# Optimization experiments

Measured on AMD Instinct MI355X. Metric: run time of the kernel, lower is better.

Reference implementation:

```python
import jax, jax.numpy as jnp
import numpy as np

DS_DIM = 2
N_EXPERTS = 64
N_CLASSES = 26
IMG = 68
BATCH = 8192
FLAT = 1960  # 10 * 14 * 14 after two conv+pool stages


def _conv2d(x, w, b):
    # x: [B, Cin, H, W], w: [Cout, Cin, kh, kw]
    y = jax.lax.conv_general_dilated(
        x, w, window_strides=(1, 1), padding='VALID',
        dimension_numbers=('NCHW', 'OIHW', 'NCHW'))
    return y + b[None, :, None, None]


def _maxpool2(x):
    return jax.lax.reduce_window(
        x, -jnp.inf, jax.lax.max,
        window_dimensions=(1, 1, 2, 2), window_strides=(1, 1, 2, 2),
        padding='VALID')


def setup_inputs() -> dict:
    key = jax.random.key(0)
    ks = jax.random.split(key, 14)
    x = jax.random.normal(ks[0], (BATCH, DS_DIM), dtype=jnp.float32)
    cls_idx = jax.random.randint(ks[1], (BATCH,), 0, N_CLASSES)
    images = jax.random.normal(ks[2], (N_CLASSES, 1, IMG, IMG), dtype=jnp.float32)
    s = 0.05
    conv1_w = jax.random.normal(ks[3], (5, 1, 5, 5), dtype=jnp.float32) * s
    conv1_b = jax.random.normal(ks[4], (5,), dtype=jnp.float32) * s
    conv2_w = jax.random.normal(ks[5], (10, 5, 5, 5), dtype=jnp.float32) * s
    conv2_b = jax.random.normal(ks[6], (10,), dtype=jnp.float32) * s
    fc1_w = jax.random.normal(ks[7], (500, FLAT + DS_DIM), dtype=jnp.float32) * s
    fc1_b = jax.random.normal(ks[8], (500,), dtype=jnp.float32) * s
    fc2_w = jax.random.normal(ks[9], (N_EXPERTS, 500), dtype=jnp.float32) * s
    fc2_b = jax.random.normal(ks[10], (N_EXPERTS,), dtype=jnp.float32) * s
    # geotorch-constrained expert matrices: B_A positive-semidefinite, C_A skew
    raw_b = jax.random.normal(ks[11], (N_EXPERTS, DS_DIM, DS_DIM), dtype=jnp.float32)
    A_B = jnp.einsum('nik,njk->nij', raw_b, raw_b) * 0.1        # PSD
    raw_c = jax.random.normal(ks[12], (N_EXPERTS, DS_DIM, DS_DIM), dtype=jnp.float32)
    A_C = (raw_c - jnp.swapaxes(raw_c, -1, -2)) * 0.5            # skew
    x_tar = jax.random.normal(ks[13], (1, DS_DIM), dtype=jnp.float32)
    return {'x': x, 'cls_idx': cls_idx, 'images': images,
            'conv1_w': conv1_w, 'conv1_b': conv1_b,
            'conv2_w': conv2_w, 'conv2_b': conv2_b,
            'fc1_w': fc1_w, 'fc1_b': fc1_b,
            'fc2_w': fc2_w, 'fc2_b': fc2_b,
            'A_B': A_B, 'A_C': A_C, 'x_tar': x_tar}


def reference(x, cls_idx, images, conv1_w, conv1_b, conv2_w, conv2_b,
              fc1_w, fc1_b, fc2_w, fc2_b, A_B, A_C, x_tar):
    # gating CNN: gather per-sample image by class index
    img = images[cls_idx]                             # [B, 1, 68, 68]
    h = _maxpool2(jax.nn.relu(_conv2d(img, conv1_w, conv1_b)))   # [B, 5, 32, 32]
    h = _maxpool2(jax.nn.relu(_conv2d(h, conv2_w, conv2_b)))     # [B, 10, 14, 14]
    h = h.reshape(h.shape[0], -1)                     # [B, 1960]
    h = jnp.concatenate([h, x], axis=1)               # [B, 1962]
    h = jax.nn.relu(h @ fc1_w.T + fc1_b)              # [B, 500]
    w_all = jax.nn.softmax(h @ fc2_w.T + fc2_b, axis=1)  # [B, N]
    # fused expert weighted-sum (original: python loop over N tiny matmuls)
    A = A_B + A_C                                     # [N, d, d]
    diff = x_tar - x                                  # [B, d]
    s_all = jnp.einsum('bn,nij,bj->bi', w_all, A, diff)
    return s_all
```

## Files before the change

### kernel.cpp

```cpp
#include <hip/hip_runtime.h>

#define WS_SC1    0
#define WS_FEAT   133120
#define WS_FC1P   184080
#define WS_FC2P   197080
#define WS_AFLAT  229080
#define WS_WX     229336

__global__ __launch_bounds__(256) void k_conv1(
    const float* __restrict__ images, const float* __restrict__ c1w,
    const float* __restrict__ c1b, const float* __restrict__ fc2w,
    const float* __restrict__ fc1w, const float* __restrict__ A_B,
    const float* __restrict__ A_C, float* __restrict__ ws)
{
    const int b = blockIdx.x, t = threadIdx.x;
    if (b >= 520) {
        if (b == 520) {
            float* P = ws + WS_FC2P;
            for (int i = t; i < 8000; i += 256) {
                int j4 = i >> 6, e = i & 63;
                float4 v;
                v.x = fc2w[e * 500 + 4 * j4 + 0];
                v.y = fc2w[e * 500 + 4 * j4 + 1];
                v.z = fc2w[e * 500 + 4 * j4 + 2];
                v.w = fc2w[e * 500 + 4 * j4 + 3];
                *(float4*)&P[i * 4] = v;
            }
        } else {
            float* Af = ws + WS_AFLAT;
            if (t < 256) Af[t] = A_B[t] + A_C[t];
            float* Wx = ws + WS_WX;
            for (int i = t; i < 1000; i += 256) {
                int j = i >> 1, k = i & 1;
                Wx[i] = fc1w[j * 1962 + 1960 + k];
            }
            float* fp = ws + WS_FC1P;
            for (int i = t; i < 13000; i += 256) fp[i] = 0.f;
        }
        return;
    }

    const int c = b / 20, r = b - c * 20;
    const int oc = r >> 2, g = r & 3;
    const int py = g * 8 + (t >> 5), px = t & 31;

    float wr[25];
#pragma unroll
    for (int i = 0; i < 25; ++i) wr[i] = c1w[oc * 25 + i];
    const float bias = c1b[oc];

    const float* im = images + c * 4624 + (2 * py) * 68 + 2 * px;
    float ir[6][6];
#pragma unroll
    for (int a = 0; a < 6; ++a)
#pragma unroll
        for (int q = 0; q < 3; ++q) {
            float2 v = *(const float2*)&im[a * 68 + 2 * q];
            ir[a][2 * q] = v.x; ir[a][2 * q + 1] = v.y;
        }

    float a00 = bias, a01 = bias, a10 = bias, a11 = bias;
#pragma unroll
    for (int ky = 0; ky < 5; ++ky)
#pragma unroll
        for (int kx = 0; kx < 5; ++kx) {
            float w = wr[ky * 5 + kx];
            a00 += w * ir[ky][kx];     a01 += w * ir[ky][kx + 1];
            a10 += w * ir[ky + 1][kx]; a11 += w * ir[ky + 1][kx + 1];
        }
    float v = fmaxf(fmaxf(fmaxf(a00, a01), fmaxf(a10, a11)), 0.f);
    ws[WS_SC1 + ((c * 5 + oc) * 32 + py) * 32 + px] = v;
}

__global__ __launch_bounds__(256) void k_conv2(
    const float* __restrict__ c2w, const float* __restrict__ c2b,
    float* __restrict__ ws)
{
    const int b = blockIdx.x, t = threadIdx.x;
    const int c = b / 10, oc = b - c * 10;

    __shared__ float sw[125];
    if (t < 125) sw[t] = c2w[oc * 125 + t];
    __syncthreads();
    if (t >= 196) return;

    const int py = t / 14, px = t - py * 14;
    const float bias = c2b[oc];
    float a00 = bias, a01 = bias, a10 = bias, a11 = bias;

    const float* base = ws + WS_SC1 + c * 5120 + (2 * py) * 32 + 2 * px;
#pragma unroll
    for (int ic = 0; ic < 5; ++ic) {
        const float* s1 = base + ic * 1024;
        float ir[6][6];
#pragma unroll
        for (int a = 0; a < 6; ++a)
#pragma unroll
            for (int q = 0; q < 3; ++q) {
                float2 v = *(const float2*)&s1[a * 32 + 2 * q];
                ir[a][2 * q] = v.x; ir[a][2 * q + 1] = v.y;
            }
#pragma unroll
        for (int ky = 0; ky < 5; ++ky)
#pragma unroll
            for (int kx = 0; kx < 5; ++kx) {
                float w = sw[ic * 25 + ky * 5 + kx];
                a00 += w * ir[ky][kx];     a01 += w * ir[ky][kx + 1];
                a10 += w * ir[ky + 1][kx]; a11 += w * ir[ky + 1][kx + 1];
            }
    }
    float v = fmaxf(fmaxf(fmaxf(a00, a01), fmaxf(a10, a11)), 0.f);
    ws[WS_FEAT + c * 1960 + oc * 196 + py * 14 + px] = v;
}

__global__ __launch_bounds__(256) void k_fc1(
    const float* __restrict__ fc1w, const float* __restrict__ fc1b,
    float* __restrict__ ws)
{
    const int lane = threadIdx.x & 63, w = threadIdx.x >> 6;
    const int jg = blockIdx.x >> 1, half = blockIdx.x & 1;
    const int j = jg * 4 + w;
    const int kbase = half * 980;

    float wreg[16];
#pragma unroll
    for (int i = 0; i < 16; ++i) {
        int kl = lane + 64 * i;
        wreg[i] = (kl < 980) ? fc1w[j * 1962 + kbase + kl] : 0.f;
    }
    const float bj = (half == 0) ? fc1b[j] : 0.f;
    const float* feat = ws + WS_FEAT;
    float* fc1p = ws + WS_FC1P;

    for (int c = 0; c < 26; ++c) {
        const float* f = feat + c * 1960 + kbase;
        float acc0 = 0.f, acc1 = 0.f;
#pragma unroll
        for (int i = 0; i < 16; i += 2) {
            int k0 = lane + 64 * i, k1 = lane + 64 * (i + 1);
            acc0 += wreg[i]     * f[(k0 < 980) ? k0 : 0];
            acc1 += wreg[i + 1] * f[(k1 < 980) ? k1 : 0];
        }
        float acc = acc0 + acc1;
#pragma unroll
        for (int off = 32; off >= 1; off >>= 1) acc += __shfl_xor(acc, off);
        if (lane == 0) atomicAdd(&fc1p[c * 500 + j], acc + bj);
    }
}

__global__ __launch_bounds__(256) void k_moe(
    const float* __restrict__ x, const int* __restrict__ cls,
    const float* __restrict__ fc2b, const float* __restrict__ x_tar,
    const float* __restrict__ ws, float* __restrict__ out)
{
    __shared__ float sh[8][500];
    __shared__ float sred[2048];
    const int t = threadIdx.x;
    const int b0 = blockIdx.x * 8;
    const float* fc1p = ws + WS_FC1P;
    const float* fc2P = ws + WS_FC2P;
    const float* Af   = ws + WS_AFLAT;
    const float* Wx   = ws + WS_WX;

    int cs[8]; float xs0[8], xs1[8];
#pragma unroll
    for (int s = 0; s < 8; ++s) {
        cs[s]  = cls[b0 + s];
        xs0[s] = x[2 * (b0 + s)];
        xs1[s] = x[2 * (b0 + s) + 1];
    }
    for (int j = t; j < 500; j += 256) {
        float2 wx = *(const float2*)&Wx[2 * j];
#pragma unroll
        for (int s = 0; s < 8; ++s) {
            float v = fc1p[cs[s] * 500 + j] + xs0[s] * wx.x + xs1[s] * wx.y;
            sh[s][j] = fmaxf(v, 0.f);
        }
    }
    __syncthreads();

    const int e = t & 63, p = t >> 6;
    float acc[8];
#pragma unroll
    for (int s = 0; s < 8; ++s) acc[s] = 0.f;

    const int gbeg = p * 32;
    const int gend = (p == 3) ? 125 : (gbeg + 32);
    for (int j4 = gbeg; j4 < gend; ++j4) {
        float4 wv = *(const float4*)&fc2P[(j4 * 64 + e) * 4];
#pragma unroll
        for (int s = 0; s < 8; ++s) {
            float4 h4 = *(const float4*)&sh[s][j4 * 4];
            acc[s] += h4.x * wv.x + h4.y * wv.y + h4.z * wv.z + h4.w * wv.w;
        }
    }
#pragma unroll
    for (int s = 0; s < 8; ++s) sred[p * 512 + s * 64 + e] = acc[s];
    __syncthreads();

    const float xt0 = x_tar[0], xt1 = x_tar[1];
    const float be = fc2b[e];
    const float4 a4 = *(const float4*)&Af[4 * e];
#pragma unroll
    for (int half = 0; half < 2; ++half) {
        int s = half * 4 + p;
        float logit = be + sred[s * 64 + e] + sred[512 + s * 64 + e]
                    + sred[1024 + s * 64 + e] + sred[1536 + s * 64 + e];
        float m = logit;
#pragma unroll
        for (int off = 32; off >= 1; off >>= 1) m = fmaxf(m, __shfl_xor(m, off));
        float ex = __expf(logit - m);
        float sum = ex;
        float m0 = ex * a4.x, m1 = ex * a4.y, m2 = ex * a4.z, m3 = ex * a4.w;
#pragma unroll
        for (int off = 32; off >= 1; off >>= 1) {
            sum += __shfl_xor(sum, off);
            m0 += __shfl_xor(m0, off);
            m1 += __shfl_xor(m1, off);
            m2 += __shfl_xor(m2, off);
            m3 += __shfl_xor(m3, off);
        }
        if (e == 0) {
            int b = b0 + s;
            float d0 = xt0 - x[2 * b], d1 = xt1 - x[2 * b + 1];
            float inv = 1.f / sum;
            out[2 * b]     = (m0 * d0 + m1 * d1) * inv;
            out[2 * b + 1] = (m2 * d0 + m3 * d1) * inv;
        }
    }
}

extern "C" void kernel_launch(void* const* d_in, const int* in_sizes, int n_in,
                              void* d_out, int out_size, void* d_ws, size_t ws_size,
                              hipStream_t stream) {
    const float* x      = (const float*)d_in[0];
    const int*   cls    = (const int*)  d_in[1];
    const float* images = (const float*)d_in[2];
    const float* c1w    = (const float*)d_in[3];
    const float* c1b    = (const float*)d_in[4];
    const float* c2w    = (const float*)d_in[5];
    const float* c2b    = (const float*)d_in[6];
    const float* fc1w   = (const float*)d_in[7];
    const float* fc1b   = (const float*)d_in[8];
    const float* fc2w   = (const float*)d_in[9];
    const float* fc2b   = (const float*)d_in[10];
    const float* A_B    = (const float*)d_in[11];
    const float* A_C    = (const float*)d_in[12];
    const float* x_tar  = (const float*)d_in[13];
    float* out = (float*)d_out;
    float* ws  = (float*)d_ws;

    k_conv1<<<522, 256, 0, stream>>>(images, c1w, c1b, fc2w, fc1w, A_B, A_C, ws);
    k_conv2<<<260, 256, 0, stream>>>(c2w, c2b, ws);
    k_fc1  <<<250, 256, 0, stream>>>(fc1w, fc1b, ws);
    k_moe  <<<1024, 256, 0, stream>>>(x, cls, fc2b, x_tar, ws, out);
}
```

Baseline: 136.2 us.

## Fuse conv1, conv2 and fc1 into one persistent kernel with grid barriers

Merges the three preprocessing kernels into a single 256-block kernel that loops over virtual blocks and separates the stages with flag-based grid barriers in workspace memory. The aim is to remove two kernel launches and the inter-kernel gaps. It depends on all 256 blocks being co-resident. The flags are never reset, so later invocations may pass the barriers early and race.

```diff
diff --git a/kernel.cpp b/kernel.cpp
--- a/kernel.cpp
+++ b/kernel.cpp
@@ -6,145 +6,155 @@
 #define WS_FC2P   197080
 #define WS_AFLAT  229080
 #define WS_WX     229336
-
-__global__ __launch_bounds__(256) void k_conv1(
-    const float* __restrict__ images, const float* __restrict__ c1w,
-    const float* __restrict__ c1b, const float* __restrict__ fc2w,
-    const float* __restrict__ fc1w, const float* __restrict__ A_B,
-    const float* __restrict__ A_C, float* __restrict__ ws)
-{
-    const int b = blockIdx.x, t = threadIdx.x;
-    if (b >= 520) {
-        if (b == 520) {
-            float* P = ws + WS_FC2P;
-            for (int i = t; i < 8000; i += 256) {
-                int j4 = i >> 6, e = i & 63;
-                float4 v;
-                v.x = fc2w[e * 500 + 4 * j4 + 0];
-                v.y = fc2w[e * 500 + 4 * j4 + 1];
-                v.z = fc2w[e * 500 + 4 * j4 + 2];
-                v.w = fc2w[e * 500 + 4 * j4 + 3];
-                *(float4*)&P[i * 4] = v;
-            }
-        } else {
-            float* Af = ws + WS_AFLAT;
-            if (t < 256) Af[t] = A_B[t] + A_C[t];
-            float* Wx = ws + WS_WX;
-            for (int i = t; i < 1000; i += 256) {
-                int j = i >> 1, k = i & 1;
-                Wx[i] = fc1w[j * 1962 + 1960 + k];
-            }
-            float* fp = ws + WS_FC1P;
-            for (int i = t; i < 13000; i += 256) fp[i] = 0.f;
-        }
-        return;
-    }
-
-    const int c = b / 20, r = b - c * 20;
-    const int oc = r >> 2, g = r & 3;
-    const int py = g * 8 + (t >> 5), px = t & 31;
-
-    float wr[25];
-#pragma unroll
-    for (int i = 0; i < 25; ++i) wr[i] = c1w[oc * 25 + i];
-    const float bias = c1b[oc];
-
-    const float* im = images + c * 4624 + (2 * py) * 68 + 2 * px;
-    float ir[6][6];
-#pragma unroll
-    for (int a = 0; a < 6; ++a)
-#pragma unroll
-        for (int q = 0; q < 3; ++q) {
-            float2 v = *(const float2*)&im[a * 68 + 2 * q];
-            ir[a][2 * q] = v.x; ir[a][2 * q + 1] = v.y;
-        }
-
-    float a00 = bias, a01 = bias, a10 = bias, a11 = bias;
-#pragma unroll
-    for (int ky = 0; ky < 5; ++ky)
-#pragma unroll
-        for (int kx = 0; kx < 5; ++kx) {
-            float w = wr[ky * 5 + kx];
-            a00 += w * ir[ky][kx];     a01 += w * ir[ky][kx + 1];
-            a10 += w * ir[ky + 1][kx]; a11 += w * ir[ky + 1][kx + 1];
-        }
-    float v = fmaxf(fmaxf(fmaxf(a00, a01), fmaxf(a10, a11)), 0.f);
-    ws[WS_SC1 + ((c * 5 + oc) * 32 + py) * 32 + px] = v;
-}
-
-__global__ __launch_bounds__(256) void k_conv2(
+#define WS_FLAGA  230336
+#define WS_FLAGB  230592
+
+#define MAGIC_A 0x5EED0001
+#define MAGIC_B 0x5EED0002
+
+__device__ __forceinline__ void grid_barrier(int* flags, int magic) {
+    __syncthreads();
+    if (threadIdx.x == 0) {
+        __hip_atomic_store(&flags[blockIdx.x], magic,
+                           __ATOMIC_RELEASE, __HIP_MEMORY_SCOPE_AGENT);
+    }
+    while (__hip_atomic_load(&flags[threadIdx.x],
+                             __ATOMIC_ACQUIRE, __HIP_MEMORY_SCOPE_AGENT) != magic) {
+        __builtin_amdgcn_s_sleep(1);
+    }
+    __syncthreads();
+}
+
+__global__ __launch_bounds__(256) void k_pre(
+    const float* __restrict__ images,
+    const float* __restrict__ c1w, const float* __restrict__ c1b,
     const float* __restrict__ c2w, const float* __restrict__ c2b,
+    const float* __restrict__ fc1w, const float* __restrict__ fc1b,
+    const float* __restrict__ fc2w,
+    const float* __restrict__ A_B, const float* __restrict__ A_C,
     float* __restrict__ ws)
 {
     const int b = blockIdx.x, t = threadIdx.x;
-    const int c = b / 10, oc = b - c * 10;
-
-    __shared__ float sw[125];
-    if (t < 125) sw[t] = c2w[oc * 125 + t];
-    __syncthreads();
-    if (t >= 196) return;
-
-    const int py = t / 14, px = t - py * 14;
-    const float bias = c2b[oc];
-    float a00 = bias, a01 = bias, a10 = bias, a11 = bias;
-
-    const float* base = ws + WS_SC1 + c * 5120 + (2 * py) * 32 + 2 * px;
-#pragma unroll
-    for (int ic = 0; ic < 5; ++ic) {
-        const float* s1 = base + ic * 1024;
+    const int g = b * 256 + t;
+
+    if (g < 8000) {
+        int j4 = g >> 6, e = g & 63;
+        float4 v;
+        v.x = fc2w[e * 500 + 4 * j4 + 0];
+        v.y = fc2w[e * 500 + 4 * j4 + 1];
+        v.z = fc2w[e * 500 + 4 * j4 + 2];
+        v.w = fc2w[e * 500 + 4 * j4 + 3];
+        *(float4*)&ws[WS_FC2P + g * 4] = v;
+    } else if (g < 8256) {
+        int i = g - 8000;
+        ws[WS_AFLAT + i] = A_B[i] + A_C[i];
+    } else if (g < 9256) {
+        int i = g - 8256, j = i >> 1, k = i & 1;
+        ws[WS_WX + i] = fc1w[j * 1962 + 1960 + k];
+    } else if (g < 22256) {
+        ws[WS_FC1P + (g - 9256)] = 0.f;
+    }
+
+    for (int vb = b; vb < 520; vb += 256) {
+        const int c = vb / 20, r = vb - c * 20;
+        const int oc = r >> 2, gg = r & 3;
+        const int py = gg * 8 + (t >> 5), px = t & 31;
+
+        float wr[25];
+#pragma unroll
+        for (int i = 0; i < 25; ++i) wr[i] = c1w[oc * 25 + i];
+        const float bias = c1b[oc];
+
+        const float* im = images + c * 4624 + (2 * py) * 68 + 2 * px;
         float ir[6][6];
 #pragma unroll
         for (int a = 0; a < 6; ++a)
 #pragma unroll
             for (int q = 0; q < 3; ++q) {
-                float2 v = *(const float2*)&s1[a * 32 + 2 * q];
+                float2 v = *(const float2*)&im[a * 68 + 2 * q];
                 ir[a][2 * q] = v.x; ir[a][2 * q + 1] = v.y;
             }
+        float a00 = bias, a01 = bias, a10 = bias, a11 = bias;
 #pragma unroll
         for (int ky = 0; ky < 5; ++ky)
 #pragma unroll
             for (int kx = 0; kx < 5; ++kx) {
-                float w = sw[ic * 25 + ky * 5 + kx];
+                float w = wr[ky * 5 + kx];
                 a00 += w * ir[ky][kx];     a01 += w * ir[ky][kx + 1];
                 a10 += w * ir[ky + 1][kx]; a11 += w * ir[ky + 1][kx + 1];
             }
-    }
-    float v = fmaxf(fmaxf(fmaxf(a00, a01), fmaxf(a10, a11)), 0.f);
-    ws[WS_FEAT + c * 1960 + oc * 196 + py * 14 + px] = v;
-}
-
-__global__ __launch_bounds__(256) void k_fc1(
-    const float* __restrict__ fc1w, const float* __restrict__ fc1b,
-    float* __restrict__ ws)
-{
-    const int lane = threadIdx.x & 63, w = threadIdx.x >> 6;
-    const int jg = blockIdx.x >> 1, half = blockIdx.x & 1;
-    const int j = jg * 4 + w;
-    const int kbase = half * 980;
-
-    float wreg[16];
-#pragma unroll
-    for (int i = 0; i < 16; ++i) {
-        int kl = lane + 64 * i;
-        wreg[i] = (kl < 980) ? fc1w[j * 1962 + kbase + kl] : 0.f;
-    }
-    const float bj = (half == 0) ? fc1b[j] : 0.f;
-    const float* feat = ws + WS_FEAT;
-    float* fc1p = ws + WS_FC1P;
-
-    for (int c = 0; c < 26; ++c) {
-        const float* f = feat + c * 1960 + kbase;
-        float acc0 = 0.f, acc1 = 0.f;
-#pragma unroll
-        for (int i = 0; i < 16; i += 2) {
-            int k0 = lane + 64 * i, k1 = lane + 64 * (i + 1);
-            acc0 += wreg[i]     * f[(k0 < 980) ? k0 : 0];
-            acc1 += wreg[i + 1] * f[(k1 < 980) ? k1 : 0];
-        }
-        float acc = acc0 + acc1;
-#pragma unroll
-        for (int off = 32; off >= 1; off >>= 1) acc += __shfl_xor(acc, off);
-        if (lane == 0) atomicAdd(&fc1p[c * 500 + j], acc + bj);
+        float v = fmaxf(fmaxf(fmaxf(a00, a01), fmaxf(a10, a11)), 0.f);
+        ws[WS_SC1 + ((c * 5 + oc) * 32 + py) * 32 + px] = v;
+    }
+
+    grid_barrier((int*)(ws + WS_FLAGA), MAGIC_A);
+
+    __shared__ float sw[125];
+    for (int vb = b; vb < 260; vb += 256) {
+        const int c = vb / 10, oc = vb - c * 10;
+        __syncthreads();
+        if (t < 125) sw[t] = c2w[oc * 125 + t];
+        __syncthreads();
+        if (t < 196) {
+            const int py = t / 14, px = t - py * 14;
+            const float bias = c2b[oc];
+            float a00 = bias, a01 = bias, a10 = bias, a11 = bias;
+            const float* base = ws + WS_SC1 + c * 5120 + (2 * py) * 32 + 2 * px;
+#pragma unroll
+            for (int ic = 0; ic < 5; ++ic) {
+                const float* s1 = base + ic * 1024;
+                float ir[6][6];
+#pragma unroll
+                for (int a = 0; a < 6; ++a)
+#pragma unroll
+                    for (int q = 0; q < 3; ++q) {
+                        float2 v = *(const float2*)&s1[a * 32 + 2 * q];
+                        ir[a][2 * q] = v.x; ir[a][2 * q + 1] = v.y;
+                    }
+#pragma unroll
+                for (int ky = 0; ky < 5; ++ky)
+#pragma unroll
+                    for (int kx = 0; kx < 5; ++kx) {
+                        float w = sw[ic * 25 + ky * 5 + kx];
+                        a00 += w * ir[ky][kx];     a01 += w * ir[ky][kx + 1];
+                        a10 += w * ir[ky + 1][kx]; a11 += w * ir[ky + 1][kx + 1];
+                    }
+            }
+            float v = fmaxf(fmaxf(fmaxf(a00, a01), fmaxf(a10, a11)), 0.f);
+            ws[WS_FEAT + c * 1960 + oc * 196 + py * 14 + px] = v;
+        }
+    }
+
+    grid_barrier((int*)(ws + WS_FLAGB), MAGIC_B);
+
+    const int lane = t & 63;
+    const int wg = b * 4 + (t >> 6);
+    if (wg < 1000) {
+        const int j = wg >> 1, half = wg & 1;
+        const int kbase = half * 980;
+        float wreg[16];
+#pragma unroll
+        for (int i = 0; i < 16; ++i) {
+            int kl = lane + 64 * i;
+            wreg[i] = (kl < 980) ? fc1w[j * 1962 + kbase + kl] : 0.f;
+        }
+        const float bj = (half == 0) ? fc1b[j] : 0.f;
+        const float* feat = ws + WS_FEAT;
+        float* fc1p = ws + WS_FC1P;
+        for (int c = 0; c < 26; ++c) {
+            const float* f = feat + c * 1960 + kbase;
+            float acc0 = 0.f, acc1 = 0.f;
+#pragma unroll
+            for (int i = 0; i < 16; i += 2) {
+                int k0 = lane + 64 * i, k1 = lane + 64 * (i + 1);
+                acc0 += wreg[i]     * f[(k0 < 980) ? k0 : 0];
+                acc1 += wreg[i + 1] * f[(k1 < 980) ? k1 : 0];
+            }
+            float acc = acc0 + acc1;
+#pragma unroll
+            for (int off = 32; off >= 1; off >>= 1) acc += __shfl_xor(acc, off);
+            if (lane == 0) atomicAdd(&fc1p[c * 500 + j], acc + bj);
+        }
     }
 }
 
@@ -221,11 +231,11 @@
             m3 += __shfl_xor(m3, off);
         }
         if (e == 0) {
-            int b = b0 + s;
-            float d0 = xt0 - x[2 * b], d1 = xt1 - x[2 * b + 1];
+            int bb = b0 + s;
+            float d0 = xt0 - x[2 * bb], d1 = xt1 - x[2 * bb + 1];
             float inv = 1.f / sum;
-            out[2 * b]     = (m0 * d0 + m1 * d1) * inv;
-            out[2 * b + 1] = (m2 * d0 + m3 * d1) * inv;
+            out[2 * bb]     = (m0 * d0 + m1 * d1) * inv;
+            out[2 * bb + 1] = (m2 * d0 + m3 * d1) * inv;
         }
     }
 }
@@ -250,8 +260,7 @@
     float* out = (float*)d_out;
     float* ws  = (float*)d_ws;
 
-    k_conv1<<<522, 256, 0, stream>>>(images, c1w, c1b, fc2w, fc1w, A_B, A_C, ws);
-    k_conv2<<<260, 256, 0, stream>>>(c2w, c2b, ws);
-    k_fc1  <<<250, 256, 0, stream>>>(fc1w, fc1b, ws);
-    k_moe  <<<1024, 256, 0, stream>>>(x, cls, fc2b, x_tar, ws, out);
-}
+    k_pre<<<256, 256, 0, stream>>>(images, c1w, c1b, c2w, c2b,
+                                   fc1w, fc1b, fc2w, A_B, A_C, ws);
+    k_moe<<<1024, 256, 0, stream>>>(x, cls, fc2b, x_tar, ws, out);
+}
```

After: 176.1 us. 1.29x slower.

## Restructure fc1 to per-class blocks with direct stores, drop atomics and zeroing

Applied to the files above, without the earlier changes.

The fc1 kernel now launches one block per (class, group of 8 outputs). Each wave computes two outputs over the full 1960-length feature vector and writes the result directly, where before each block split K in half, held weights in registers across all 26 classes and combined the halves with atomicAdd. This removes the atomics and the workspace zero-fill in the conv1 kernel and raises parallelism from 250 to 1638 blocks. In exchange, the fc1 weights are re-read from global memory once per class instead of staying in registers.

```diff
diff --git a/kernel.cpp b/kernel.cpp
--- a/kernel.cpp
+++ b/kernel.cpp
@@ -34,8 +34,6 @@
                 int j = i >> 1, k = i & 1;
                 Wx[i] = fc1w[j * 1962 + 1960 + k];
             }
-            float* fp = ws + WS_FC1P;
-            for (int i = t; i < 13000; i += 256) fp[i] = 0.f;
         }
         return;
     }
@@ -118,33 +116,39 @@
     float* __restrict__ ws)
 {
     const int lane = threadIdx.x & 63, w = threadIdx.x >> 6;
-    const int jg = blockIdx.x >> 1, half = blockIdx.x & 1;
-    const int j = jg * 4 + w;
-    const int kbase = half * 980;
-
-    float wreg[16];
-#pragma unroll
-    for (int i = 0; i < 16; ++i) {
-        int kl = lane + 64 * i;
-        wreg[i] = (kl < 980) ? fc1w[j * 1962 + kbase + kl] : 0.f;
-    }
-    const float bj = (half == 0) ? fc1b[j] : 0.f;
-    const float* feat = ws + WS_FEAT;
-    float* fc1p = ws + WS_FC1P;
-
-    for (int c = 0; c < 26; ++c) {
-        const float* f = feat + c * 1960 + kbase;
-        float acc0 = 0.f, acc1 = 0.f;
-#pragma unroll
-        for (int i = 0; i < 16; i += 2) {
-            int k0 = lane + 64 * i, k1 = lane + 64 * (i + 1);
-            acc0 += wreg[i]     * f[(k0 < 980) ? k0 : 0];
-            acc1 += wreg[i + 1] * f[(k1 < 980) ? k1 : 0];
-        }
-        float acc = acc0 + acc1;
-#pragma unroll
-        for (int off = 32; off >= 1; off >>= 1) acc += __shfl_xor(acc, off);
-        if (lane == 0) atomicAdd(&fc1p[c * 500 + j], acc + bj);
+    const int c = blockIdx.x / 63, jg = blockIdx.x - c * 63;
+    const int j0 = jg * 8 + 2 * w;
+    if (j0 >= 500) return;
+    const int j1 = j0 + 1;
+
+    const float* f  = ws + WS_FEAT + c * 1960;
+    const float* w0 = fc1w + j0 * 1962;
+    const float* w1 = fc1w + j1 * 1962;
+
+    float acc0 = 0.f, acc1 = 0.f;
+#pragma unroll
+    for (int i = 0; i < 30; ++i) {
+        int k = lane + 64 * i;
+        float fv = f[k];
+        acc0 += w0[k] * fv;
+        acc1 += w1[k] * fv;
+    }
+    {
+        int k = lane + 1920;
+        if (k < 1960) {
+            float fv = f[k];
+            acc0 += w0[k] * fv;
+            acc1 += w1[k] * fv;
+        }
+    }
+#pragma unroll
+    for (int off = 32; off >= 1; off >>= 1) {
+        acc0 += __shfl_xor(acc0, off);
+        acc1 += __shfl_xor(acc1, off);
+    }
+    if (lane == 0) {
+        ws[WS_FC1P + c * 500 + j0] = acc0 + fc1b[j0];
+        ws[WS_FC1P + c * 500 + j1] = acc1 + fc1b[j1];
     }
 }
 
@@ -221,11 +225,11 @@
             m3 += __shfl_xor(m3, off);
         }
         if (e == 0) {
-            int b = b0 + s;
-            float d0 = xt0 - x[2 * b], d1 = xt1 - x[2 * b + 1];
+            int bb = b0 + s;
+            float d0 = xt0 - x[2 * bb], d1 = xt1 - x[2 * bb + 1];
             float inv = 1.f / sum;
-            out[2 * b]     = (m0 * d0 + m1 * d1) * inv;
-            out[2 * b + 1] = (m2 * d0 + m3 * d1) * inv;
+            out[2 * bb]     = (m0 * d0 + m1 * d1) * inv;
+            out[2 * bb + 1] = (m2 * d0 + m3 * d1) * inv;
         }
     }
 }
@@ -252,6 +256,6 @@
 
     k_conv1<<<522, 256, 0, stream>>>(images, c1w, c1b, fc2w, fc1w, A_B, A_C, ws);
     k_conv2<<<260, 256, 0, stream>>>(c2w, c2b, ws);
-    k_fc1  <<<250, 256, 0, stream>>>(fc1w, fc1b, ws);
+    k_fc1  <<<1638, 256, 0, stream>>>(fc1w, fc1b, ws);
     k_moe  <<<1024, 256, 0, stream>>>(x, cls, fc2b, x_tar, ws, out);
 }
```

After: 129.5 us. -4.9%, faster.
